# Optimization experiments

Hardware: AMD Instinct MI355X
Metric: run time of the kernel (lower is better)

## Reference

```python
import jax, jax.numpy as jnp
import numpy as np

# NF4 codebook (bitsandbytes normal-float-4 values)
NF4 = jnp.asarray(np.array([
    -1.0, -0.6961928009986877, -0.5250730514526367, -0.39491748809814453,
    -0.28444138169288635, -0.18477343022823334, -0.09105003625154495, 0.0,
    0.07958029955625534, 0.16093020141124725, 0.24611230194568634, 0.33791524171829224,
    0.44070982933044434, 0.5626170039176941, 0.7229568362236023, 1.0], dtype=np.float32))

BLOCK = 64         # bnb nf4 blocksize
SCALING = 2.0      # alpha / r = 128 / 64
OUT, IN = 4096, 4096

def dequantize_nf4(codes, absmax):
    # codes: [out, in] int32 in [0,16); absmax: [out*in/BLOCK] per-block scale
    vals = NF4[codes].reshape(-1, BLOCK)           # [n_blocks, BLOCK]
    w = vals * absmax[:, None]                     # blockwise rescale
    return w.reshape(OUT, IN)                      # [out, in]

def setup_inputs() -> dict:
    key = jax.random.key(0)
    k1, k2, k3, k4, k5 = jax.random.split(key, 5)
    x = jax.random.normal(k1, (4, 2048, 4096), dtype=jnp.float32)
    lora_A = jax.random.normal(k2, (64, 4096), dtype=jnp.float32) * 0.02
    lora_B = jax.random.normal(k3, (4096, 64), dtype=jnp.float32) * 0.02
    absmax = jax.random.uniform(k4, (4096 * 4096 // BLOCK,), dtype=jnp.float32) * 0.1
    qweight_codes = jax.random.randint(k5, (4096, 4096), 0, 16, dtype=jnp.int32)
    return {"x": x, "lora_A": lora_A, "lora_B": lora_B,
            "absmax": absmax, "qweight_codes": qweight_codes}

def reference(x, lora_A, lora_B, absmax, qweight_codes):
    # LinearForward, quantized nf4 path, no dora/bone, dropout disabled (eval):
    # F.linear(x, W) + scaling * F.linear(F.linear(x, lora_A), lora_B)
    W = dequantize_nf4(qweight_codes, absmax)              # [out, in]
    base = jnp.einsum('btd,od->bto', x, W)                 # base GEMM
    lora = jnp.einsum('btr,or->bto', jnp.einsum('btd,rd->btr', x, lora_A), lora_B)
    return base + SCALING * lora
```

## Files before the change

### kernel.cpp

```cpp
#include <hip/hip_runtime.h>


typedef _Float16 half8 __attribute__((ext_vector_type(8)));
typedef float f32x4 __attribute__((ext_vector_type(4)));

#define M_DIM 8192
#define N_DIM 4096
#define K_DIM 4096
#define NT (K_DIM / 64)

__constant__ float NF4C[16] = {
    -1.0f, -0.6961928009986877f, -0.5250730514526367f, -0.39491748809814453f,
    -0.28444138169288635f, -0.18477343022823334f, -0.09105003625154495f, 0.0f,
    0.07958029955625534f, 0.16093020141124725f, 0.24611230194568634f, 0.33791524171829224f,
    0.44070982933044434f, 0.5626170039176941f, 0.7229568362236023f, 1.0f};

__device__ __forceinline__ void gl16(void* lds, const void* g) {
  __builtin_amdgcn_global_load_lds(
      (const __attribute__((address_space(1))) void*)g,
      (__attribute__((address_space(3))) void*)lds, 16, 0, 0);
}

__global__ __launch_bounds__(256) void prep_x(const float4* __restrict__ x,
                                              half8* __restrict__ xh) {
  size_t i = (size_t)blockIdx.x * 256 + threadIdx.x;
  float4 a = x[2 * i];
  float4 b = x[2 * i + 1];
  half8 h;
  h[0] = (_Float16)a.x; h[1] = (_Float16)a.y; h[2] = (_Float16)a.z; h[3] = (_Float16)a.w;
  h[4] = (_Float16)b.x; h[5] = (_Float16)b.y; h[6] = (_Float16)b.z; h[7] = (_Float16)b.w;
  xh[i] = h;
}

#define PWP 132
__global__ __launch_bounds__(256) void prep_w(const float* __restrict__ lora_A,
                                              const float* __restrict__ lora_B,
                                              const float* __restrict__ absmax,
                                              const int* __restrict__ codes,
                                              _Float16* __restrict__ Wc) {
  __shared__ float At[64 * PWP];
  __shared__ float Bt[64 * PWP];
  __shared__ float nf4s[16];
  const int tid = threadIdx.x;
  const int bxi = blockIdx.x & 31;
  const int byo = blockIdx.x >> 5;
  const int i0 = bxi * 128;
  const int o0 = byo * 128;
  if (tid < 16) nf4s[tid] = NF4C[tid];
  for (int idx = tid; idx < 8192; idx += 256) {
    int r = idx >> 7, ii = idx & 127;
    At[r * PWP + ii] = lora_A[(size_t)r * 4096 + i0 + ii];
  }
  for (int idx = tid; idx < 8192; idx += 256) {
    int oo = idx >> 6, r = idx & 63;
    Bt[r * PWP + oo] = lora_B[(size_t)(o0 + oo) * 64 + r];
  }
  __syncthreads();
  const int tx = tid & 15;
  const int ty = tid >> 4;
  float accw[8][8];
#pragma unroll
  for (int i = 0; i < 8; ++i)
#pragma unroll
    for (int j = 0; j < 8; ++j) accw[i][j] = 0.0f;
  for (int r = 0; r < 64; ++r) {
    float4 a0 = *(const float4*)&At[r * PWP + tx * 8];
    float4 a1 = *(const float4*)&At[r * PWP + tx * 8 + 4];
    float4 b0 = *(const float4*)&Bt[r * PWP + ty * 8];
    float4 b1 = *(const float4*)&Bt[r * PWP + ty * 8 + 4];
    float av[8] = {a0.x, a0.y, a0.z, a0.w, a1.x, a1.y, a1.z, a1.w};
    float bv[8] = {b0.x, b0.y, b0.z, b0.w, b1.x, b1.y, b1.z, b1.w};
#pragma unroll
    for (int i = 0; i < 8; ++i)
#pragma unroll
      for (int j = 0; j < 8; ++j) accw[i][j] += bv[i] * av[j];
  }
#pragma unroll
  for (int i = 0; i < 8; ++i) {
    const int o_g = o0 + ty * 8 + i;
    const int* crow = codes + (size_t)o_g * 4096 + i0 + tx * 8;
    int4 c0 = *(const int4*)crow;
    int4 c1 = *(const int4*)(crow + 4);
    const float am = absmax[o_g * 64 + (i0 >> 6) + (tx >> 3)];
    half8 h;
    h[0] = (_Float16)(nf4s[c0.x] * am + 2.0f * accw[i][0]);
    h[1] = (_Float16)(nf4s[c0.y] * am + 2.0f * accw[i][1]);
    h[2] = (_Float16)(nf4s[c0.z] * am + 2.0f * accw[i][2]);
    h[3] = (_Float16)(nf4s[c0.w] * am + 2.0f * accw[i][3]);
    h[4] = (_Float16)(nf4s[c1.x] * am + 2.0f * accw[i][4]);
    h[5] = (_Float16)(nf4s[c1.y] * am + 2.0f * accw[i][5]);
    h[6] = (_Float16)(nf4s[c1.z] * am + 2.0f * accw[i][6]);
    h[7] = (_Float16)(nf4s[c1.w] * am + 2.0f * accw[i][7]);
    *(half8*)(Wc + (size_t)o_g * 4096 + i0 + tx * 8) = h;
  }
}


#define BAR __builtin_amdgcn_s_barrier()
#define LGKM0 asm volatile("s_waitcnt lgkmcnt(0)" ::: "memory")

__global__ __launch_bounds__(512, 2) void gemm(const _Float16* __restrict__ Xh,
                                               const _Float16* __restrict__ Wc,
                                               float* __restrict__ out) {
  __shared__ _Float16 lds[65536];
  const int tid = threadIdx.x;
  const int lane = tid & 63;
  const int w = tid >> 6;

  const int swz = (blockIdx.x & 7) * 64 + (blockIdx.x >> 3);
  const int by = swz >> 4;
  const int bx = swz & 15;

  const int m16 = lane & 15;
  const int quad = lane >> 4;
  const int csw = (quad ^ (m16 & 7)) * 8;
  const int aoff0 = m16 * 64 + csw;
  const int aoff1 = m16 * 64 + (csw ^ 32);
  const int ha = w >> 2;
  const int hboff = ((w & 3) >> 1) * 8192 + (w & 1) * 4096;

  const int r0 = tid >> 3;
  const int lc = (tid & 7) ^ (r0 & 7);
  const _Float16* gAbase = Xh + (size_t)(by * 256 + r0) * K_DIM + lc * 8;
  const _Float16* gBbase = Wc + (size_t)(bx * 256 + r0) * K_DIM + lc * 8;

#define STAGE_A(H, BUF, T)                                                   \
  do {                                                                       \
    _Float16* d_ = lds + (BUF) * 32768 + (H) * 8192 + w * 512;               \
    const _Float16* s_ = gAbase + (size_t)((H) * 128) * K_DIM + (T) * 64;    \
    gl16(d_, s_);                                                            \
    gl16(d_ + 4096, s_ + (size_t)64 * K_DIM);                                \
  } while (0)
#define STAGE_B(H, BUF, T)                                                   \
  do {                                                                       \
    _Float16* d_ = lds + (BUF) * 32768 + 16384 + (H) * 8192 + w * 512;       \
    const _Float16* s_ = gBbase + (size_t)((H) * 128) * K_DIM + (T) * 64;    \
    gl16(d_, s_);                                                            \
    gl16(d_ + 4096, s_ + (size_t)64 * K_DIM);                                \
  } while (0)

  f32x4 acc[8][4];
#pragma unroll
  for (int m = 0; m < 8; ++m)
#pragma unroll
    for (int n = 0; n < 4; ++n) acc[m][n] = (f32x4){0.f, 0.f, 0.f, 0.f};

  half8 af[4][2];
  half8 bf[2][2];

#define LOAD_A(MH)                                                           \
  do {                                                                       \
    _Pragma("unroll") for (int fm = 0; fm < 4; ++fm) {                       \
      af[fm][0] = *(const half8*)(rA + (MH) * 4096 + fm * 1024 + aoff0);     \
      af[fm][1] = *(const half8*)(rA + (MH) * 4096 + fm * 1024 + aoff1);     \
    }                                                                        \
  } while (0)
#define LOAD_B(NH)                                                           \
  do {                                                                       \
    _Pragma("unroll") for (int fn = 0; fn < 2; ++fn) {                       \
      bf[fn][0] = *(const half8*)(rBw + (NH) * 2048 + fn * 1024 + aoff0);    \
      bf[fn][1] = *(const half8*)(rBw + (NH) * 2048 + fn * 1024 + aoff1);    \
    }                                                                        \
  } while (0)
#define MFMA16(MH, NH)                                                       \
  do {                                                                       \
    __builtin_amdgcn_s_setprio(1);                                           \
    _Pragma("unroll") for (int fm = 0; fm < 4; ++fm)                         \
        _Pragma("unroll") for (int fn = 0; fn < 2; ++fn) {                   \
      acc[(MH) * 4 + fm][(NH) * 2 + fn] = __builtin_amdgcn_mfma_f32_16x16x32_f16( \
          af[fm][0], bf[fn][0], acc[(MH) * 4 + fm][(NH) * 2 + fn], 0, 0, 0); \
      acc[(MH) * 4 + fm][(NH) * 2 + fn] = __builtin_amdgcn_mfma_f32_16x16x32_f16( \
          af[fm][1], bf[fn][1], acc[(MH) * 4 + fm][(NH) * 2 + fn], 0, 0, 0); \
    }                                                                        \
    __builtin_amdgcn_s_setprio(0);                                           \
  } while (0)

  STAGE_A(0, 0, 0);
  STAGE_A(1, 0, 0);
  STAGE_B(0, 0, 0);
  STAGE_B(1, 0, 0);
  STAGE_A(0, 1, 1);
  asm volatile("s_waitcnt vmcnt(2)" ::: "memory");
  BAR;

  for (int t = 0; t < NT; ++t) {
    const int bsel = t & 1;
    const int bn = bsel ^ 1;
    const _Float16* rA = lds + bsel * 32768 + ha * 8192;
    const _Float16* rBw = lds + bsel * 32768 + 16384 + hboff;
    const bool more1 = (t + 1 < NT);
    LOAD_A(0);
    LOAD_B(0);
    if (more1) STAGE_A(1, bn, t + 1);
    BAR; LGKM0;
    MFMA16(0, 0);
    BAR;
    LOAD_B(1);
    if (more1) STAGE_B(0, bn, t + 1);
    BAR; LGKM0;
    MFMA16(0, 1);
    BAR;
    LOAD_A(1);
    if (more1) STAGE_B(1, bn, t + 1);
    BAR; LGKM0;
    MFMA16(1, 1);
    BAR;
    LOAD_B(0);
    if (t + 2 < NT) {
      STAGE_A(0, bsel, t + 2);
      asm volatile("s_waitcnt vmcnt(2)" ::: "memory");
    } else {
      asm volatile("s_waitcnt vmcnt(0)" ::: "memory");
    }
    BAR; LGKM0;
    MFMA16(1, 0);
    BAR;
  }

  const size_t rowbase = (size_t)by * 256 + ha * 128 + quad * 4;
  const int colbase = bx * 256 + (w & 3) * 64 + m16;
#pragma unroll
  for (int m = 0; m < 8; ++m) {
#pragma unroll
    for (int r = 0; r < 4; ++r) {
      float* po = out + (rowbase + m * 16 + r) * N_DIM + colbase;
      po[0]  = acc[m][0][r];
      po[16] = acc[m][1][r];
      po[32] = acc[m][2][r];
      po[48] = acc[m][3][r];
    }
  }
}

extern "C" void kernel_launch(void* const* d_in, const int* in_sizes, int n_in,
                              void* d_out, int out_size, void* d_ws, size_t ws_size,
                              hipStream_t stream) {
  const float* x      = (const float*)d_in[0];
  const float* lora_A = (const float*)d_in[1];
  const float* lora_B = (const float*)d_in[2];
  const float* absmax = (const float*)d_in[3];
  const int*   codes  = (const int*)d_in[4];
  float* out = (float*)d_out;

  _Float16* Xh = (_Float16*)d_ws;
  _Float16* Wc = Xh + (size_t)M_DIM * K_DIM;

  hipLaunchKernelGGL(prep_x, dim3((M_DIM * K_DIM) / (8 * 256)), dim3(256), 0, stream,
                     (const float4*)x, (half8*)Xh);
  hipLaunchKernelGGL(prep_w, dim3((N_DIM / 128) * (K_DIM / 128)), dim3(256), 0, stream,
                     lora_A, lora_B, absmax, codes, Wc);
  hipLaunchKernelGGL(gemm, dim3((M_DIM / 256) * (N_DIM / 256)), dim3(512), 0, stream,
                     Xh, Wc, out);
}
```

Measured before the change: 522.3 us.

## Interleave LDS fragment reads with MFMAs via staged lgkmcnt waits and unrolled tiles

Restructures the GEMM main loop into a TILE macro that is unrolled by two with compile-time buffer indices. Each phase now waits on partial lgkmcnt counts, fenced by sched_barrier, so MFMAs on the first fragments can start while later LDS reads are still in flight. The loop previously waited for all LDS reads to finish before any MFMA. The global-to-LDS loads for the next tile (A half 1 and both B halves) are all issued in the first phase instead of being spread over three phases. This front-loads memory traffic and makes the vmcnt accounting more intricate, in exchange for removing per-iteration buffer-select arithmetic and improving overlap of LDS latency with matrix math.

```diff
diff --git a/kernel.cpp b/kernel.cpp
--- a/kernel.cpp
+++ b/kernel.cpp
@@ -15,10 +15,10 @@
     0.07958029955625534f, 0.16093020141124725f, 0.24611230194568634f, 0.33791524171829224f,
     0.44070982933044434f, 0.5626170039176941f, 0.7229568362236023f, 1.0f};
 
-__device__ __forceinline__ void gl16(void* lds, const void* g) {
+__device__ __forceinline__ void gl16(void* lds_p, const void* g) {
   __builtin_amdgcn_global_load_lds(
       (const __attribute__((address_space(1))) void*)g,
-      (__attribute__((address_space(3))) void*)lds, 16, 0, 0);
+      (__attribute__((address_space(3))) void*)lds_p, 16, 0, 0);
 }
 
 __global__ __launch_bounds__(256) void prep_x(const float4* __restrict__ x,
@@ -97,7 +97,18 @@
 
 
 #define BAR __builtin_amdgcn_s_barrier()
-#define LGKM0 asm volatile("s_waitcnt lgkmcnt(0)" ::: "memory")
+#define PRIO1 __builtin_amdgcn_s_setprio(1)
+#define PRIO0 __builtin_amdgcn_s_setprio(0)
+#define SB0 __builtin_amdgcn_sched_barrier(0)
+
+#define VMC_(N) asm volatile("s_waitcnt vmcnt(" #N ")" ::: "memory")
+#define VMC(N) VMC_(N)
+#define LG_(N)                                              \
+  do {                                                      \
+    asm volatile("s_waitcnt lgkmcnt(" #N ")" ::: "memory"); \
+    __builtin_amdgcn_sched_barrier(0);                      \
+  } while (0)
+#define LG(N) LG_(N)
 
 __global__ __launch_bounds__(512, 2) void gemm(const _Float16* __restrict__ Xh,
                                                const _Float16* __restrict__ Wc,
@@ -124,19 +135,19 @@
   const _Float16* gAbase = Xh + (size_t)(by * 256 + r0) * K_DIM + lc * 8;
   const _Float16* gBbase = Wc + (size_t)(bx * 256 + r0) * K_DIM + lc * 8;
 
-#define STAGE_A(H, BUF, T)                                                   \
-  do {                                                                       \
-    _Float16* d_ = lds + (BUF) * 32768 + (H) * 8192 + w * 512;               \
-    const _Float16* s_ = gAbase + (size_t)((H) * 128) * K_DIM + (T) * 64;    \
-    gl16(d_, s_);                                                            \
-    gl16(d_ + 4096, s_ + (size_t)64 * K_DIM);                                \
-  } while (0)
-#define STAGE_B(H, BUF, T)                                                   \
-  do {                                                                       \
-    _Float16* d_ = lds + (BUF) * 32768 + 16384 + (H) * 8192 + w * 512;       \
-    const _Float16* s_ = gBbase + (size_t)((H) * 128) * K_DIM + (T) * 64;    \
-    gl16(d_, s_);                                                            \
-    gl16(d_ + 4096, s_ + (size_t)64 * K_DIM);                                \
+#define STAGE_A(H, BUF, T)                                                \
+  do {                                                                    \
+    _Float16* d_ = lds + (BUF) * 32768 + (H) * 8192 + w * 512;            \
+    const _Float16* s_ = gAbase + (size_t)((H) * 128) * K_DIM + (T) * 64; \
+    gl16(d_, s_);                                                         \
+    gl16(d_ + 4096, s_ + (size_t)64 * K_DIM);                             \
+  } while (0)
+#define STAGE_B(H, BUF, T)                                                \
+  do {                                                                    \
+    _Float16* d_ = lds + (BUF) * 32768 + 16384 + (H) * 8192 + w * 512;    \
+    const _Float16* s_ = gBbase + (size_t)((H) * 128) * K_DIM + (T) * 64; \
+    gl16(d_, s_);                                                         \
+    gl16(d_ + 4096, s_ + (size_t)64 * K_DIM);                             \
   } while (0)
 
   f32x4 acc[8][4];
@@ -148,31 +159,94 @@
   half8 af[4][2];
   half8 bf[2][2];
 
-#define LOAD_A(MH)                                                           \
+#define RDA(FM, P)                                          \
+  do {                                                      \
+    af[FM][0] = *(const half8*)((P) + (FM)*1024 + aoff0);   \
+    af[FM][1] = *(const half8*)((P) + (FM)*1024 + aoff1);   \
+  } while (0)
+#define RDB(FN, P)                                          \
+  do {                                                      \
+    bf[FN][0] = *(const half8*)((P) + (FN)*1024 + aoff0);   \
+    bf[FN][1] = *(const half8*)((P) + (FN)*1024 + aoff1);   \
+  } while (0)
+
+#define MFM(FM, MH, NH)                                                      \
   do {                                                                       \
-    _Pragma("unroll") for (int fm = 0; fm < 4; ++fm) {                       \
-      af[fm][0] = *(const half8*)(rA + (MH) * 4096 + fm * 1024 + aoff0);     \
-      af[fm][1] = *(const half8*)(rA + (MH) * 4096 + fm * 1024 + aoff1);     \
-    }                                                                        \
-  } while (0)
-#define LOAD_B(NH)                                                           \
-  do {                                                                       \
-    _Pragma("unroll") for (int fn = 0; fn < 2; ++fn) {                       \
-      bf[fn][0] = *(const half8*)(rBw + (NH) * 2048 + fn * 1024 + aoff0);    \
-      bf[fn][1] = *(const half8*)(rBw + (NH) * 2048 + fn * 1024 + aoff1);    \
-    }                                                                        \
-  } while (0)
-#define MFMA16(MH, NH)                                                       \
-  do {                                                                       \
-    __builtin_amdgcn_s_setprio(1);                                           \
-    _Pragma("unroll") for (int fm = 0; fm < 4; ++fm)                         \
-        _Pragma("unroll") for (int fn = 0; fn < 2; ++fn) {                   \
-      acc[(MH) * 4 + fm][(NH) * 2 + fn] = __builtin_amdgcn_mfma_f32_16x16x32_f16( \
-          af[fm][0], bf[fn][0], acc[(MH) * 4 + fm][(NH) * 2 + fn], 0, 0, 0); \
-      acc[(MH) * 4 + fm][(NH) * 2 + fn] = __builtin_amdgcn_mfma_f32_16x16x32_f16( \
-          af[fm][1], bf[fn][1], acc[(MH) * 4 + fm][(NH) * 2 + fn], 0, 0, 0); \
-    }                                                                        \
-    __builtin_amdgcn_s_setprio(0);                                           \
+    acc[(MH)*4 + (FM)][(NH)*2 + 0] = __builtin_amdgcn_mfma_f32_16x16x32_f16( \
+        af[FM][0], bf[0][0], acc[(MH)*4 + (FM)][(NH)*2 + 0], 0, 0, 0);       \
+    acc[(MH)*4 + (FM)][(NH)*2 + 0] = __builtin_amdgcn_mfma_f32_16x16x32_f16( \
+        af[FM][1], bf[0][1], acc[(MH)*4 + (FM)][(NH)*2 + 0], 0, 0, 0);       \
+    acc[(MH)*4 + (FM)][(NH)*2 + 1] = __builtin_amdgcn_mfma_f32_16x16x32_f16( \
+        af[FM][0], bf[1][0], acc[(MH)*4 + (FM)][(NH)*2 + 1], 0, 0, 0);       \
+    acc[(MH)*4 + (FM)][(NH)*2 + 1] = __builtin_amdgcn_mfma_f32_16x16x32_f16( \
+        af[FM][1], bf[1][1], acc[(MH)*4 + (FM)][(NH)*2 + 1], 0, 0, 0);       \
+  } while (0)
+
+#define MFN(FN, MH, NH)                                                          \
+  do {                                                                           \
+    _Pragma("unroll") for (int fm_ = 0; fm_ < 4; ++fm_) {                        \
+      acc[(MH)*4 + fm_][(NH)*2 + (FN)] = __builtin_amdgcn_mfma_f32_16x16x32_f16( \
+          af[fm_][0], bf[FN][0], acc[(MH)*4 + fm_][(NH)*2 + (FN)], 0, 0, 0);     \
+      acc[(MH)*4 + fm_][(NH)*2 + (FN)] = __builtin_amdgcn_mfma_f32_16x16x32_f16( \
+          af[fm_][1], bf[FN][1], acc[(MH)*4 + fm_][(NH)*2 + (FN)], 0, 0, 0);     \
+    }                                                                            \
+  } while (0)
+
+#define TILE(BUF, T, S1, S4, VW)                                        \
+  do {                                                                  \
+    const _Float16* rA = lds + (BUF)*32768 + ha * 8192;                 \
+    const _Float16* rB = lds + (BUF)*32768 + 16384 + hboff;             \
+                                     \
+    RDB(0, rB); RDB(1, rB); RDA(0, rA);                                 \
+    SB0;                                                                \
+    RDA(1, rA); RDA(2, rA); RDA(3, rA);                                 \
+    if (S1) {                                                           \
+      STAGE_A(1, (BUF) ^ 1, (T) + 1);                                   \
+      STAGE_B(0, (BUF) ^ 1, (T) + 1);                                   \
+      STAGE_B(1, (BUF) ^ 1, (T) + 1);                                   \
+    }                                                                   \
+    BAR;                                                                \
+    PRIO1;                                                              \
+    LG(6); MFM(0, 0, 0);                                                \
+    LG(4); MFM(1, 0, 0);                                                \
+    LG(2); MFM(2, 0, 0);                                                \
+    LG(0); MFM(3, 0, 0);                                                \
+    PRIO0;                                                              \
+    BAR;                                                                \
+                                              \
+    RDB(0, rB + 2048);                                                  \
+    SB0;                                                                \
+    RDB(1, rB + 2048);                                                  \
+    BAR;                                                                \
+    PRIO1;                                                              \
+    LG(2); MFN(0, 0, 1);                                                \
+    LG(0); MFN(1, 0, 1);                                                \
+    PRIO0;                                                              \
+    BAR;                                                                \
+                                              \
+    RDA(0, rA + 4096);                                                  \
+    SB0;                                                                \
+    RDA(1, rA + 4096); RDA(2, rA + 4096); RDA(3, rA + 4096);            \
+    BAR;                                                                \
+    PRIO1;                                                              \
+    LG(6); MFM(0, 1, 1);                                                \
+    LG(4); MFM(1, 1, 1);                                                \
+    LG(2); MFM(2, 1, 1);                                                \
+    LG(0); MFM(3, 1, 1);                                                \
+    PRIO0;                                                              \
+    BAR;                                                                \
+     \
+    RDB(0, rB);                                                         \
+    SB0;                                                                \
+    RDB(1, rB);                                                         \
+    if (S4) STAGE_A(0, BUF, (T) + 2);                                   \
+    BAR;                                                                \
+    PRIO1;                                                              \
+    LG(2); MFN(0, 1, 0);                                                \
+    LG(0); MFN(1, 1, 0);                                                \
+    PRIO0;                                                              \
+    VMC(VW);                                                            \
+    BAR;                                                                \
   } while (0)
 
   STAGE_A(0, 0, 0);
@@ -180,42 +254,15 @@
   STAGE_B(0, 0, 0);
   STAGE_B(1, 0, 0);
   STAGE_A(0, 1, 1);
-  asm volatile("s_waitcnt vmcnt(2)" ::: "memory");
+  VMC(2);
   BAR;
 
-  for (int t = 0; t < NT; ++t) {
-    const int bsel = t & 1;
-    const int bn = bsel ^ 1;
-    const _Float16* rA = lds + bsel * 32768 + ha * 8192;
-    const _Float16* rBw = lds + bsel * 32768 + 16384 + hboff;
-    const bool more1 = (t + 1 < NT);
-    LOAD_A(0);
-    LOAD_B(0);
-    if (more1) STAGE_A(1, bn, t + 1);
-    BAR; LGKM0;
-    MFMA16(0, 0);
-    BAR;
-    LOAD_B(1);
-    if (more1) STAGE_B(0, bn, t + 1);
-    BAR; LGKM0;
-    MFMA16(0, 1);
-    BAR;
-    LOAD_A(1);
-    if (more1) STAGE_B(1, bn, t + 1);
-    BAR; LGKM0;
-    MFMA16(1, 1);
-    BAR;
-    LOAD_B(0);
-    if (t + 2 < NT) {
-      STAGE_A(0, bsel, t + 2);
-      asm volatile("s_waitcnt vmcnt(2)" ::: "memory");
-    } else {
-      asm volatile("s_waitcnt vmcnt(0)" ::: "memory");
-    }
-    BAR; LGKM0;
-    MFMA16(1, 0);
-    BAR;
-  }
+  for (int t2 = 0; t2 < NT - 2; t2 += 2) {
+    TILE(0, t2, 1, 1, 2);
+    TILE(1, t2 + 1, 1, 1, 2);
+  }
+  TILE(0, NT - 2, 1, 0, 0);
+  TILE(1, NT - 1, 0, 0, 0);
 
   const size_t rowbase = (size_t)by * 256 + ha * 128 + quad * 4;
   const int colbase = bx * 256 + (w & 3) * 64 + m16;
```

Result: no change. 529.1 us (+1.3%).
